# Optimization experiments

Hardware: AMD Instinct MI355X
Metric: run time of the kernel (lower is better)

The kernel has to match this reference:

```python
import jax, jax.numpy as jnp
import numpy as np

M, K, N = 4096, 4096, 11008  # tokens, in_features, out_features


def setup_inputs() -> dict:
    key = jax.random.key(0)
    k0, k1, k2 = jax.random.split(key, 3)
    # quint8 activations: values in [0, 255], zero_point 128
    x_q = jax.random.randint(k0, (M, K), 0, 256, dtype=jnp.int32)
    # qint8 weight: values in [-128, 127], zero_point 0 (as prepacked in __init__)
    w_q = jax.random.randint(k1, (N, K), -128, 128, dtype=jnp.int32)
    bias = jax.random.normal(k2, (N,), dtype=jnp.float32) * 0.1
    return {
        "x_q": x_q,
        "w_q": w_q,
        "bias": bias,
        "x_scale": jnp.float32(0.02),
        "w_scale": jnp.float32(0.01),
        "out_scale": jnp.float32(1.0),   # self.scale = 1.0
        "x_zero_point": 128,
        "out_zero_point": 0,             # self.zero_point = 0
    }


def reference(x_q, w_q, bias, x_scale, w_scale, out_scale, x_zero_point, out_zero_point):
    # int8 GEMM with int32 accumulation: (x - zp_x) @ W^T
    acc = jnp.einsum(
        "mk,nk->mn",
        x_q - x_zero_point,
        w_q,
        preferred_element_type=jnp.int32,
    )
    # dequantize + bias (fp32), then requantize to quint8 output
    y = acc.astype(jnp.float32) * (x_scale * w_scale) + bias
    q = jnp.clip(jnp.round(y / out_scale) + out_zero_point, 0, 255).astype(jnp.int32)
    return q
```

## Files before the change

### kernel.cpp

```cpp
#include <hip/hip_runtime.h>

#define M_DIM 4096
#define K_DIM 4096
#define N_DIM 11008
#define BM 128
#define BN 128
#define BK 64

typedef int v4i __attribute__((ext_vector_type(4)));

__device__ __forceinline__ void load_lds16(const void* g, void* l) {
    __builtin_amdgcn_global_load_lds(
        (const __attribute__((address_space(1))) void*)g,
        (__attribute__((address_space(3))) void*)l,
        16, 0, 0);
}

__global__ void pack_x_kernel(const int* __restrict__ x, signed char* __restrict__ out,
                              const int* __restrict__ zp_p, int n4) {
    int i = blockIdx.x * blockDim.x + threadIdx.x;
    if (i >= n4) return;
    int zp = zp_p[0];
    int4 v = ((const int4*)x)[i];
    unsigned int p = ((unsigned int)(v.x - zp) & 0xFF)
                   | (((unsigned int)(v.y - zp) & 0xFF) << 8)
                   | (((unsigned int)(v.z - zp) & 0xFF) << 16)
                   | (((unsigned int)(v.w - zp) & 0xFF) << 24);
    ((unsigned int*)out)[i] = p;
}

__global__ void pack_w_kernel(const int* __restrict__ w, signed char* __restrict__ out, int n4) {
    int i = blockIdx.x * blockDim.x + threadIdx.x;
    if (i >= n4) return;
    int4 v = ((const int4*)w)[i];
    unsigned int p = ((unsigned int)v.x & 0xFF)
                   | (((unsigned int)v.y & 0xFF) << 8)
                   | (((unsigned int)v.z & 0xFF) << 16)
                   | (((unsigned int)v.w & 0xFF) << 24);
    ((unsigned int*)out)[i] = p;
}

__global__ __launch_bounds__(256) void gemm_i8_kernel(
    const signed char* __restrict__ A8,
    const signed char* __restrict__ B8,
    const float* __restrict__ bias,
    const float* __restrict__ xs_p, const float* __restrict__ ws_p,
    const float* __restrict__ os_p, const int* __restrict__ ozp_p,
    int* __restrict__ out) {
    __shared__ v4i As[BM * BK / 16];
    __shared__ v4i Bs[BN * BK / 16];

    const int tid  = threadIdx.x;
    const int lane = tid & 63;
    const int wave = tid >> 6;
    const int m0 = blockIdx.y * BM;
    const int n0 = blockIdx.x * BN;

    const int s0 = tid, s1 = tid + 256;
    const int row0 = s0 >> 2, row1 = s1 >> 2;
    const int g0 = (s0 & 3) ^ ((row0 >> 2) & 3);
    const int g1 = (s1 & 3) ^ ((row1 >> 2) & 3);
    const long offA0 = (long)(m0 + row0) * K_DIM + g0 * 16;
    const long offA1 = (long)(m0 + row1) * K_DIM + g1 * 16;
    const long offB0 = (long)(n0 + row0) * K_DIM + g0 * 16;
    const long offB1 = (long)(n0 + row1) * K_DIM + g1 * 16;
    char* ldsA0 = (char*)As + s0 * 16;
    char* ldsA1 = (char*)As + s1 * 16;
    char* ldsB0 = (char*)Bs + s0 * 16;
    char* ldsB1 = (char*)Bs + s1 * 16;

    const int waveM = wave >> 1, waveN = wave & 1;
    const int l15 = lane & 15, quad = lane >> 4;
    const int sw = l15 >> 2;
    int aSlot[4], bSlot[4];
#pragma unroll
    for (int t = 0; t < 4; ++t) {
        aSlot[t] = (waveM * 64 + t * 16 + l15) * 4 + (quad ^ sw);
        bSlot[t] = (waveN * 64 + t * 16 + l15) * 4 + (quad ^ sw);
    }

    v4i acc[4][4];
#pragma unroll
    for (int mt = 0; mt < 4; ++mt)
#pragma unroll
        for (int nt = 0; nt < 4; ++nt) {
            v4i z = {0, 0, 0, 0};
            acc[mt][nt] = z;
        }

    for (int k0 = 0; k0 < K_DIM; k0 += BK) {
        load_lds16(A8 + offA0 + k0, ldsA0);
        load_lds16(A8 + offA1 + k0, ldsA1);
        load_lds16(B8 + offB0 + k0, ldsB0);
        load_lds16(B8 + offB1 + k0, ldsB1);
        __syncthreads();

        v4i a[4], b[4];
#pragma unroll
        for (int t = 0; t < 4; ++t) a[t] = As[aSlot[t]];
#pragma unroll
        for (int t = 0; t < 4; ++t) b[t] = Bs[bSlot[t]];
#pragma unroll
        for (int mt = 0; mt < 4; ++mt)
#pragma unroll
            for (int nt = 0; nt < 4; ++nt)
                acc[mt][nt] = __builtin_amdgcn_mfma_i32_16x16x64_i8(
                    a[mt], b[nt], acc[mt][nt], 0, 0, 0);
        __syncthreads();
    }

    const float scale  = xs_p[0] * ws_p[0];
    const float inv_os = 1.0f / os_p[0];
    const int   ozp    = ozp_p[0];
#pragma unroll
    for (int mt = 0; mt < 4; ++mt) {
        const int rbase = m0 + waveM * 64 + mt * 16 + quad * 4;
#pragma unroll
        for (int nt = 0; nt < 4; ++nt) {
            const int col = n0 + waveN * 64 + nt * 16 + l15;
            const float bv = bias[col];
#pragma unroll
            for (int r = 0; r < 4; ++r) {
                float y = (float)acc[mt][nt][r] * scale + bv;
                int q = (int)rintf(y * inv_os) + ozp;
                q = q < 0 ? 0 : (q > 255 ? 255 : q);
                out[(long)(rbase + r) * N_DIM + col] = q;
            }
        }
    }
}

extern "C" void kernel_launch(void* const* d_in, const int* in_sizes, int n_in,
                              void* d_out, int out_size, void* d_ws, size_t ws_size,
                              hipStream_t stream) {
    const int*   x_q  = (const int*)d_in[0];
    const int*   w_q  = (const int*)d_in[1];
    const float* bias = (const float*)d_in[2];
    const float* xs   = (const float*)d_in[3];
    const float* wsc  = (const float*)d_in[4];
    const float* os   = (const float*)d_in[5];
    const int*   xzp  = (const int*)d_in[6];
    const int*   ozp  = (const int*)d_in[7];

    signed char* x8 = (signed char*)d_ws;
    signed char* w8 = (signed char*)d_ws + (size_t)M_DIM * K_DIM;

    const int nx4 = M_DIM * K_DIM / 4;
    pack_x_kernel<<<(nx4 + 255) / 256, 256, 0, stream>>>(x_q, x8, xzp, nx4);
    const int nw4 = N_DIM * K_DIM / 4;
    pack_w_kernel<<<(nw4 + 255) / 256, 256, 0, stream>>>(w_q, w8, nw4);

    dim3 grid(N_DIM / BN, M_DIM / BM);
    gemm_i8_kernel<<<grid, 256, 0, stream>>>(x8, w8, bias, xs, wsc, os, ozp, (int*)d_out);
}
```

Before: 594.8 us.

## Double K tile to 128 and remap blocks for XCD-aware L2 locality

Doubles the K-step per iteration so each barrier pair covers twice the MFMA work, with a wider 8-way XOR swizzle on the LDS layout. It also switches to a 1D grid with an XCD-aware block mapping, so blocks on the same XCD share 4x4 groups of M/N tiles and reuse A/B rows in L2. The larger tile doubles LDS use to 32KB per block, which may reduce occupancy. The mapping assumes 32 M-blocks and 86 N-blocks fit the chosen decomposition.

```diff
diff --git a/kernel.cpp b/kernel.cpp
--- a/kernel.cpp
+++ b/kernel.cpp
@@ -5,7 +5,7 @@
 #define N_DIM 11008
 #define BM 128
 #define BN 128
-#define BK 64
+#define BK 128
 
 typedef int v4i __attribute__((ext_vector_type(4)));
 
@@ -53,30 +53,39 @@
     const int tid  = threadIdx.x;
     const int lane = tid & 63;
     const int wave = tid >> 6;
-    const int m0 = blockIdx.y * BM;
-    const int n0 = blockIdx.x * BN;
 
-    const int s0 = tid, s1 = tid + 256;
-    const int row0 = s0 >> 2, row1 = s1 >> 2;
-    const int g0 = (s0 & 3) ^ ((row0 >> 2) & 3);
-    const int g1 = (s1 & 3) ^ ((row1 >> 2) & 3);
-    const long offA0 = (long)(m0 + row0) * K_DIM + g0 * 16;
-    const long offA1 = (long)(m0 + row1) * K_DIM + g1 * 16;
-    const long offB0 = (long)(n0 + row0) * K_DIM + g0 * 16;
-    const long offB1 = (long)(n0 + row1) * K_DIM + g1 * 16;
-    char* ldsA0 = (char*)As + s0 * 16;
-    char* ldsA1 = (char*)As + s1 * 16;
-    char* ldsB0 = (char*)Bs + s0 * 16;
-    char* ldsB1 = (char*)Bs + s1 * 16;
+    const int bid   = blockIdx.x;
+    const int xcd   = bid & 7;
+    const int local = bid >> 3;
+    const int m_blk = xcd * 4 + (local & 3);
+    const int n_blk = (local >> 4) * 4 + ((local & 15) >> 2);
+    const int m0 = m_blk * BM;
+    const int n0 = n_blk * BN;
+
+    long offA[4], offB[4];
+    char *ldsA[4], *ldsB[4];
+#pragma unroll
+    for (int j = 0; j < 4; ++j) {
+        const int s   = tid + 256 * j;
+        const int row = s >> 3;
+        const int gg  = (s & 7) ^ (row & 7);
+        offA[j] = (long)(m0 + row) * K_DIM + gg * 16;
+        offB[j] = (long)(n0 + row) * K_DIM + gg * 16;
+        ldsA[j] = (char*)As + s * 16;
+        ldsB[j] = (char*)Bs + s * 16;
+    }
 
     const int waveM = wave >> 1, waveN = wave & 1;
     const int l15 = lane & 15, quad = lane >> 4;
-    const int sw = l15 >> 2;
-    int aSlot[4], bSlot[4];
+    int aSlot[4][2], bSlot[4][2];
 #pragma unroll
     for (int t = 0; t < 4; ++t) {
-        aSlot[t] = (waveM * 64 + t * 16 + l15) * 4 + (quad ^ sw);
-        bSlot[t] = (waveN * 64 + t * 16 + l15) * 4 + (quad ^ sw);
+#pragma unroll
+        for (int ks = 0; ks < 2; ++ks) {
+            const int g = ks * 4 + quad;
+            aSlot[t][ks] = (waveM * 64 + t * 16 + l15) * 8 + (g ^ (l15 & 7));
+            bSlot[t][ks] = (waveN * 64 + t * 16 + l15) * 8 + (g ^ (l15 & 7));
+        }
     }
 
     v4i acc[4][4];
@@ -89,23 +98,26 @@
         }
 
     for (int k0 = 0; k0 < K_DIM; k0 += BK) {
-        load_lds16(A8 + offA0 + k0, ldsA0);
-        load_lds16(A8 + offA1 + k0, ldsA1);
-        load_lds16(B8 + offB0 + k0, ldsB0);
-        load_lds16(B8 + offB1 + k0, ldsB1);
+#pragma unroll
+        for (int j = 0; j < 4; ++j) load_lds16(A8 + offA[j] + k0, ldsA[j]);
+#pragma unroll
+        for (int j = 0; j < 4; ++j) load_lds16(B8 + offB[j] + k0, ldsB[j]);
         __syncthreads();
 
-        v4i a[4], b[4];
 #pragma unroll
-        for (int t = 0; t < 4; ++t) a[t] = As[aSlot[t]];
+        for (int ks = 0; ks < 2; ++ks) {
+            v4i a[4], b[4];
 #pragma unroll
-        for (int t = 0; t < 4; ++t) b[t] = Bs[bSlot[t]];
+            for (int t = 0; t < 4; ++t) a[t] = As[aSlot[t][ks]];
 #pragma unroll
-        for (int mt = 0; mt < 4; ++mt)
+            for (int t = 0; t < 4; ++t) b[t] = Bs[bSlot[t][ks]];
 #pragma unroll
-            for (int nt = 0; nt < 4; ++nt)
-                acc[mt][nt] = __builtin_amdgcn_mfma_i32_16x16x64_i8(
-                    a[mt], b[nt], acc[mt][nt], 0, 0, 0);
+            for (int mt = 0; mt < 4; ++mt)
+#pragma unroll
+                for (int nt = 0; nt < 4; ++nt)
+                    acc[mt][nt] = __builtin_amdgcn_mfma_i32_16x16x64_i8(
+                        a[mt], b[nt], acc[mt][nt], 0, 0, 0);
+        }
         __syncthreads();
     }
 
@@ -150,6 +162,6 @@
     const int nw4 = N_DIM * K_DIM / 4;
     pack_w_kernel<<<(nw4 + 255) / 256, 256, 0, stream>>>(w_q, w8, nw4);
 
-    dim3 grid(N_DIM / BN, M_DIM / BM);
-    gemm_i8_kernel<<<grid, 256, 0, stream>>>(x8, w8, bias, xs, wsc, os, ozp, (int*)d_out);
+    const int nblocks = (M_DIM / BM) * (N_DIM / BN);
+    gemm_i8_kernel<<<nblocks, 256, 0, stream>>>(x8, w8, bias, xs, wsc, os, ozp, (int*)d_out);
 }
```

After: 565.9 us. -4.9%, faster.
